# Performance work log

Hardware: AMD Instinct MI355X
Metric: run time of the kernel (lower is better)

## Reference

```python
import jax, jax.numpy as jnp
import numpy as np

STRIDE = 1
PADDING = 1  # zeros padding mode

def setup_inputs() -> dict:
    key = jax.random.key(0)
    k1, k2, k3 = jax.random.split(key, 3)
    N, C_in, H, W = 32, 128, 56, 56
    C_out, kH, kW = 256, 3, 3
    x = jax.random.normal(k1, (N, C_in, H, W), dtype=jnp.float32)
    fan_in = C_in * kH * kW
    weight = jax.random.normal(k2, (C_out, C_in, kH, kW), dtype=jnp.float32) / np.sqrt(fan_in)
    bias = jax.random.normal(k3, (C_out,), dtype=jnp.float32) * 0.01
    return {"x": x, "weight": weight, "bias": bias}

def reference(x, weight, bias):
    # Same math as the im2col unfold + GEMM: a standard 2D cross-correlation
    # with zero padding. Expressed as the fused implicit-GEMM conv primitive.
    out = jax.lax.conv_general_dilated(
        x, weight,
        window_strides=(STRIDE, STRIDE),
        padding=[(PADDING, PADDING), (PADDING, PADDING)],
        dimension_numbers=("NCHW", "OIHW", "NCHW"),
    )
    # bias broadcast over (N, C_out, H_out, W_out)
    return out + bias[None, :, None, None]
```

## Files before the change

kernel.cpp:

```cpp
#include <hip/hip_runtime.h>


typedef __attribute__((ext_vector_type(8))) short short8;
typedef __attribute__((ext_vector_type(4))) float float4v;

constexpr int NB = 32, CI = 128, HH = 56, WW = 56, CO = 256;
constexpr int HWP = HH * WW;
constexpr int HP = 58, WP = 58;
constexpr size_t XTP_BYTES = (size_t)NB * HP * WP * CI * 2;
constexpr size_t WT_OFF    = XTP_BYTES;
constexpr size_t WT_BYTES  = (size_t)9 * CO * CI * 2;
constexpr size_t WS_NEED   = WT_OFF + WT_BYTES;

__device__ inline ushort f2bf(float v) {
    union { float f; uint u; } c; c.f = v;
    uint u = c.u;
    return (ushort)((u + 0x7fffu + ((u >> 16) & 1u)) >> 16);
}

__device__ inline void gll(const ushort* g, ushort* l) {
    __builtin_amdgcn_global_load_lds(
        (const __attribute__((address_space(1))) uint*)g,
        (__attribute__((address_space(3))) uint*)l, 16, 0, 0);
}

#define BAR() do { asm volatile("" ::: "memory"); \
                   __builtin_amdgcn_s_barrier(); \
                   asm volatile("" ::: "memory"); } while (0)

__global__ __launch_bounds__(256) void xform_x(const float* __restrict__ x,
                                               ushort* __restrict__ xTp) {
    int b = blockIdx.x;
    int cit = b & 3;
    int hwt = (b >> 2) % 49;
    int n   = b / (4 * 49);
    int ci0 = cit * 32, hw0 = hwt * 64;
    __shared__ float t[32][65];
    int tx = threadIdx.x;
    int col = tx & 63, r4 = tx >> 6;
#pragma unroll
    for (int rr = 0; rr < 8; ++rr) {
        int row = rr * 4 + r4;
        t[row][col] = x[((size_t)n * CI + ci0 + row) * HWP + hw0 + col];
    }
    __syncthreads();
    int i = tx & 31, j0 = tx >> 5;
#pragma unroll
    for (int jj = 0; jj < 8; ++jj) {
        int j = jj * 8 + j0;
        int hw = hw0 + j;
        int h = hw / WW, w = hw % WW;
        xTp[(((size_t)n * HP + h + 1) * WP + (w + 1)) * CI + ci0 + i] = f2bf(t[i][j]);
    }
}

__global__ __launch_bounds__(256) void xform_border(ushort* __restrict__ xTp) {
    int u = blockIdx.x * 256 + threadIdx.x;
    int ci8 = u & 15;
    int r = u >> 4;
    int n = r / 228, bb = r % 228;
    int hp, wp;
    if (bb < 58)       { hp = 0;  wp = bb; }
    else if (bb < 116) { hp = 57; wp = bb - 58; }
    else { int c = bb - 116; hp = 1 + (c >> 1); wp = (c & 1) * 57; }
    short8 z = (short8)0;
    *reinterpret_cast<short8*>(xTp + (((size_t)n * HP + hp) * WP + wp) * CI + ci8 * 8) = z;
}

__global__ __launch_bounds__(256) void xform_w(const float* __restrict__ w,
                                               ushort* __restrict__ wT) {
    int o = blockIdx.x * 256 + threadIdx.x;
    int ci = o & 127;
    int co = (o >> 7) & 255;
    int tap = o >> 15;
    wT[o] = f2bf(w[((size_t)co * CI + ci) * 9 + tap]);
}

__global__ __launch_bounds__(512, 2) void gemm_conv(
    const ushort* __restrict__ xTp, const ushort* __restrict__ wT,
    const float* __restrict__ bias, float* __restrict__ out)
{
    __shared__ ushort As[2][256 * 64];
    __shared__ ushort Bs[2][256 * 64];

    int b = blockIdx.x;
    const int mblk = (b & 7) * 49 + (b >> 3);

    const int tid = threadIdx.x, lane = tid & 63, wv = tid >> 6;
    const int wr = wv >> 2;
    const int wc = wv & 3;

    const int s8 = (((tid & 7) ^ ((tid >> 3) & 7))) * 8;
    const int aSrc = (tid >> 3) * CI + s8;
    const int dstOff = (tid >> 3) * 64 + (tid & 7) * 8;

    int bPix[4];
#pragma unroll
    for (int hq = 0; hq < 4; ++hq) {
        int m = mblk * 256 + (hq >> 1) * 128 + (hq & 1) * 64 + (tid >> 3);
        int n = m / HWP, hw = m % HWP, h = hw / WW, w = hw % WW;
        bPix[hq] = ((n * HP + h + 1) * WP + (w + 1)) * CI + s8;
    }

    const int ck0 = (((lane >> 4)) ^ (lane & 7)) * 8;
    const int ck1 = ((4 + (lane >> 4)) ^ (lane & 7)) * 8;
    const int aRowOff = (wr * 128 + (lane & 15)) * 64;
    const int bRowOff = (wc * 64 + (lane & 15)) * 64;

    float4v acc[8][4];
#pragma unroll
    for (int i = 0; i < 8; ++i)
#pragma unroll
        for (int j = 0; j < 4; ++j) acc[i][j] = (float4v)(0.0f);

    short8 aF[4][2];
    short8 bQ0[2][2];
    short8 bQ1[2][2];

    auto STAGE_A = [&](int buf, int t, int h) {
        int tap = t >> 1, kh = (t & 1) * 64;
        const ushort* src = wT + aSrc + tap * (CO * CI) + kh + h * 16384;
        ushort* dst = &As[buf][h * 8192 + dstOff];
        gll(src, dst);
        gll(src + 8192, dst + 4096);
    };
    auto STAGE_B = [&](int buf, int t, int h) {
        int tap = t >> 1, kh = (t & 1) * 64;
        int dh = tap / 3 - 1, dw = tap % 3 - 1;
        int toff = (dh * WP + dw) * CI + kh;
        ushort* dst = &Bs[buf][h * 8192 + dstOff];
        gll(xTp + bPix[h * 2 + 0] + toff, dst);
        gll(xTp + bPix[h * 2 + 1] + toff, dst + 4096);
    };
    auto LDA = [&](int buf, int qr) {
        const ushort* p = &As[buf][aRowOff + qr * 4096];
#pragma unroll
        for (int fi = 0; fi < 4; ++fi) {
            aF[fi][0] = *(const short8*)(p + fi * 1024 + ck0);
            aF[fi][1] = *(const short8*)(p + fi * 1024 + ck1);
        }
    };
    auto LDB = [&](int buf, int qc, short8 (&bF)[2][2]) {
        const ushort* p = &Bs[buf][bRowOff + qc * 2048];
#pragma unroll
        for (int gi = 0; gi < 2; ++gi) {
            bF[gi][0] = *(const short8*)(p + gi * 1024 + ck0);
            bF[gi][1] = *(const short8*)(p + gi * 1024 + ck1);
        }
    };

#define MMQ(QR, QC, BF) do { \
    __builtin_amdgcn_s_setprio(1); \
    _Pragma("unroll") \
    for (int kc = 0; kc < 2; ++kc) \
        _Pragma("unroll") \
        for (int fi = 0; fi < 4; ++fi) \
            _Pragma("unroll") \
            for (int gi = 0; gi < 2; ++gi) \
                acc[(QR)*4+fi][(QC)*2+gi] = __builtin_amdgcn_mfma_f32_16x16x32_bf16( \
                    aF[fi][kc], (BF)[gi][kc], acc[(QR)*4+fi][(QC)*2+gi], 0, 0, 0); \
    __builtin_amdgcn_s_setprio(0); \
} while (0)

    auto TILE = [&](int c, int t) {
        LDA(c, 0);
        LDB(c, 0, bQ0);
        if (t + 1 < 18) STAGE_A(c ^ 1, t + 1, 1);
        BAR();
        MMQ(0, 0, bQ0);
        LDB(c, 1, bQ1);
        if (t + 1 < 18) STAGE_B(c ^ 1, t + 1, 1);
        BAR();
        MMQ(0, 1, bQ1);
        LDA(c, 1);
        if (t + 2 < 18) STAGE_B(c, t + 2, 0);
        BAR();
        MMQ(1, 1, bQ1);
        if (t + 2 < 18) STAGE_A(c, t + 2, 0);
        BAR();
        MMQ(1, 0, bQ0);
        if (t <= 15)      { asm volatile("s_waitcnt vmcnt(4)" ::: "memory"); }
        else if (t == 16) { asm volatile("s_waitcnt vmcnt(0)" ::: "memory"); }
        BAR();
    };

    STAGE_A(0, 0, 0); STAGE_A(0, 0, 1);
    STAGE_B(0, 0, 0); STAGE_B(0, 0, 1);
    STAGE_B(1, 1, 0); STAGE_A(1, 1, 0);
    asm volatile("s_waitcnt vmcnt(4)" ::: "memory");
    BAR();

#pragma unroll 1
    for (int tp = 0; tp < 18; tp += 2) {
        TILE(0, tp);
        TILE(1, tp + 1);
    }
#undef MMQ

    const int co0 = wr * 128;
    const int m0  = mblk * 256 + wc * 64;
    float bv[8][4];
#pragma unroll
    for (int f = 0; f < 8; ++f)
#pragma unroll
        for (int r = 0; r < 4; ++r)
            bv[f][r] = bias[co0 + f * 16 + (lane >> 4) * 4 + r];
#pragma unroll
    for (int g = 0; g < 4; ++g) {
        int m = m0 + g * 16 + (lane & 15);
        int n = m / HWP, hw = m % HWP;
        float* obase = out + (size_t)n * CO * HWP + hw;
#pragma unroll
        for (int f = 0; f < 8; ++f) {
            int co = co0 + f * 16 + (lane >> 4) * 4;
#pragma unroll
            for (int r = 0; r < 4; ++r)
                obase[(size_t)(co + r) * HWP] = acc[f][g][r] + bv[f][r];
        }
    }
}

__global__ __launch_bounds__(256) void conv_k(
    const float* __restrict__ x, const float* __restrict__ wgt,
    const float* __restrict__ bias, float* __restrict__ out)
{
    int idx = blockIdx.x * 256 + threadIdx.x;
    int wg = idx % 14; int t = idx / 14;
    int ho = t % 56; t /= 56;
    int cog = t % 64; int n = t / 64;
    int w0 = wg * 4, co0 = cog * 4;
    float acc[4][4];
#pragma unroll
    for (int j = 0; j < 4; ++j) {
        float bj = bias[co0 + j];
#pragma unroll
        for (int p = 0; p < 4; ++p) acc[j][p] = bj;
    }
    const float* xn = x + (size_t)n * CI * HWP;
    for (int ci = 0; ci < CI; ++ci) {
        float xr[3][6];
#pragma unroll
        for (int kh = 0; kh < 3; ++kh) {
            int hi = ho + kh - 1;
            if (hi >= 0 && hi < HH) {
                const float* row = xn + ((size_t)ci * HH + hi) * WW;
                float4 cc = *reinterpret_cast<const float4*>(row + w0);
                xr[kh][1] = cc.x; xr[kh][2] = cc.y; xr[kh][3] = cc.z; xr[kh][4] = cc.w;
                xr[kh][0] = (w0 > 0) ? row[w0 - 1] : 0.0f;
                xr[kh][5] = (w0 + 4 < WW) ? row[w0 + 4] : 0.0f;
            } else {
#pragma unroll
                for (int q = 0; q < 6; ++q) xr[kh][q] = 0.0f;
            }
        }
#pragma unroll
        for (int j = 0; j < 4; ++j) {
            const float* wp = wgt + ((size_t)(co0 + j) * CI + ci) * 9;
            float wvv[9];
#pragma unroll
            for (int q = 0; q < 9; ++q) wvv[q] = wp[q];
#pragma unroll
            for (int kh = 0; kh < 3; ++kh)
#pragma unroll
                for (int kw = 0; kw < 3; ++kw)
#pragma unroll
                    for (int p = 0; p < 4; ++p)
                        acc[j][p] = fmaf(xr[kh][p + kw], wvv[kh * 3 + kw], acc[j][p]);
        }
    }
#pragma unroll
    for (int j = 0; j < 4; ++j) {
        float4 v = make_float4(acc[j][0], acc[j][1], acc[j][2], acc[j][3]);
        *reinterpret_cast<float4*>(out + (((size_t)n * CO + co0 + j) * HH + ho) * WW + w0) = v;
    }
}

extern "C" void kernel_launch(void* const* d_in, const int* in_sizes, int n_in,
                              void* d_out, int out_size, void* d_ws, size_t ws_size,
                              hipStream_t stream) {
    const float* x = (const float*)d_in[0];
    const float* w = (const float*)d_in[1];
    const float* b = (const float*)d_in[2];
    float* out = (float*)d_out;

    if (ws_size < WS_NEED) {
        hipLaunchKernelGGL(conv_k, dim3(6272), dim3(256), 0, stream, x, w, b, out);
        return;
    }

    ushort* xTp = (ushort*)d_ws;
    ushort* wT  = (ushort*)((char*)d_ws + WT_OFF);

    hipLaunchKernelGGL(xform_x, dim3(32 * 49 * 4), dim3(256), 0, stream, x, xTp);
    hipLaunchKernelGGL(xform_border, dim3(456), dim3(256), 0, stream, xTp);
    hipLaunchKernelGGL(xform_w, dim3(9 * CO * CI / 256), dim3(256), 0, stream, w, wT);
    hipLaunchKernelGGL(gemm_conv, dim3(392), dim3(512), 0, stream,
                       xTp, wT, b, out);
}
```

Baseline: 95.82 us.

## Stage output tile through swizzled LDS for vectorized coalesced stores; move final MFMA after barrier

The epilogue now writes accumulators plus bias into LDS in four passes, using an XOR swizzle to avoid bank conflicts. It then reads them back as float4 rows so each thread issues 16-byte stores that are contiguous along the spatial dimension, replacing the scattered scalar stores strided by HWP. It also moves the last MFMA quarter of each tile after the vmcnt wait and barrier, which changes where the memory wait overlaps compute. The epilogue gains extra barriers and LDS traffic, and the float4 stores assume a group of four pixels never crosses an image boundary (3136 is divisible by 4).

```diff
diff --git a/kernel.cpp b/kernel.cpp
--- a/kernel.cpp
+++ b/kernel.cpp
@@ -177,11 +177,10 @@
         BAR();
         MMQ(1, 1, bQ1);
         if (t + 2 < 18) STAGE_A(c, t + 2, 0);
-        BAR();
-        MMQ(1, 0, bQ0);
         if (t <= 15)      { asm volatile("s_waitcnt vmcnt(4)" ::: "memory"); }
         else if (t == 16) { asm volatile("s_waitcnt vmcnt(0)" ::: "memory"); }
         BAR();
+        MMQ(1, 0, bQ0);
     };
 
     STAGE_A(0, 0, 0); STAGE_A(0, 0, 1);
@@ -197,25 +196,46 @@
     }
 #undef MMQ
 
-    const int co0 = wr * 128;
-    const int m0  = mblk * 256 + wc * 64;
+    const int m0  = mblk * 256;
     float bv[8][4];
 #pragma unroll
     for (int f = 0; f < 8; ++f)
 #pragma unroll
         for (int r = 0; r < 4; ++r)
-            bv[f][r] = bias[co0 + f * 16 + (lane >> 4) * 4 + r];
-#pragma unroll
-    for (int g = 0; g < 4; ++g) {
-        int m = m0 + g * 16 + (lane & 15);
-        int n = m / HWP, hw = m % HWP;
-        float* obase = out + (size_t)n * CO * HWP + hw;
-#pragma unroll
-        for (int f = 0; f < 8; ++f) {
-            int co = co0 + f * 16 + (lane >> 4) * 4;
-#pragma unroll
-            for (int r = 0; r < 4; ++r)
-                obase[(size_t)(co + r) * HWP] = acc[f][g][r] + bv[f][r];
+            bv[f][r] = bias[wr * 128 + f * 16 + (lane >> 4) * 4 + r];
+
+    float* lbuf = (float*)&As[0][0];
+    const int rd_col = tid >> 3;
+    const int rd_swz = ((rd_col ^ (rd_col >> 2)) & 3) << 3;
+
+#pragma unroll 1
+    for (int q = 0; q < 4; ++q) {
+        BAR();
+        if (wr == (q >> 1)) {
+            const int fb = 4 * (q & 1);
+#pragma unroll
+            for (int f4 = 0; f4 < 4; ++f4) {
+#pragma unroll
+                for (int r = 0; r < 4; ++r) {
+                    int co_l = f4 * 16 + (lane >> 4) * 4 + r;
+                    int swz = ((co_l ^ (co_l >> 2)) & 3) << 3;
+#pragma unroll
+                    for (int g = 0; g < 4; ++g) {
+                        int ml = wc * 64 + g * 16 + (lane & 15);
+                        lbuf[co_l * 256 + (ml ^ swz)] = acc[fb + f4][g][r] + bv[fb + f4][r];
+                    }
+                }
+            }
+        }
+        BAR();
+        const int co = q * 64 + rd_col;
+#pragma unroll
+        for (int k = 0; k < 8; ++k) {
+            int ml = ((tid & 7) + 8 * k) * 4;
+            float4v v = *(const float4v*)&lbuf[rd_col * 256 + (ml ^ rd_swz)];
+            int m = m0 + ml;
+            int n = m / HWP, hw = m % HWP;
+            *(float4v*)(out + ((size_t)n * CO + co) * HWP + hw) = v;
         }
     }
 }
```

New measurement: 148.9 us. 1.55x slower.

## Retile conv GEMM to 256x224 pixel tiles aligned to four image rows

Applied to the files above, without the earlier changes.

Changes the GEMM block tile from 256 output channels by 256 pixels to 256 by 224 pixels, where each tile covers exactly four rows of one image. The warp layout becomes 4x2 with 64x112 per-warp subtiles, so each warp holds a 4x7 accumulator array. The grid grows from 392 to 448 blocks, and B staging masks off half the threads for the last 32 rows. The intent is to spread work over more blocks on the GPU's compute units and to simplify index math, since a tile never crosses an image boundary. In exchange, per-warp operand reuse drops and the B loads become uneven across threads.

```diff
diff --git a/kernel.cpp b/kernel.cpp
--- a/kernel.cpp
+++ b/kernel.cpp
@@ -81,41 +81,43 @@
     const float* __restrict__ bias, float* __restrict__ out)
 {
     __shared__ ushort As[2][256 * 64];
-    __shared__ ushort Bs[2][256 * 64];
+    __shared__ ushort Bs[2][224 * 64];
 
     int b = blockIdx.x;
-    const int mblk = (b & 7) * 49 + (b >> 3);
+    const int mblk = (b & 7) * 56 + (b >> 3);
 
     const int tid = threadIdx.x, lane = tid & 63, wv = tid >> 6;
-    const int wr = wv >> 2;
-    const int wc = wv & 3;
+    const int wr = wv >> 1;
+    const int wc = wv & 1;
 
     const int s8 = (((tid & 7) ^ ((tid >> 3) & 7))) * 8;
     const int aSrc = (tid >> 3) * CI + s8;
     const int dstOff = (tid >> 3) * 64 + (tid & 7) * 8;
 
+    const int nimg = mblk / 14;
+    const int h0   = (mblk % 14) * 4;
     int bPix[4];
 #pragma unroll
-    for (int hq = 0; hq < 4; ++hq) {
-        int m = mblk * 256 + (hq >> 1) * 128 + (hq & 1) * 64 + (tid >> 3);
-        int n = m / HWP, hw = m % HWP, h = hw / WW, w = hw % WW;
-        bPix[hq] = ((n * HP + h + 1) * WP + (w + 1)) * CI + s8;
+    for (int p = 0; p < 4; ++p) {
+        int row = p * 64 + (tid >> 3);
+        int hh = h0 + row / 56, ww2 = row % 56;
+        bPix[p] = ((nimg * HP + hh + 1) * WP + (ww2 + 1)) * CI + s8;
     }
 
     const int ck0 = (((lane >> 4)) ^ (lane & 7)) * 8;
     const int ck1 = ((4 + (lane >> 4)) ^ (lane & 7)) * 8;
-    const int aRowOff = (wr * 128 + (lane & 15)) * 64;
-    const int bRowOff = (wc * 64 + (lane & 15)) * 64;
-
-    float4v acc[8][4];
-#pragma unroll
-    for (int i = 0; i < 8; ++i)
-#pragma unroll
-        for (int j = 0; j < 4; ++j) acc[i][j] = (float4v)(0.0f);
-
-    short8 aF[4][2];
-    short8 bQ0[2][2];
-    short8 bQ1[2][2];
+    const int aRowOff = (wr * 64 + (lane & 15)) * 64;
+    const int bRowOff = (wc * 112 + (lane & 15)) * 64;
+
+    float4v acc[4][7];
+#pragma unroll
+    for (int i = 0; i < 4; ++i)
+#pragma unroll
+        for (int j = 0; j < 7; ++j) acc[i][j] = (float4v)(0.0f);
+
+    short8 aF[2][2];
+    short8 bQ0[4][2];
+    short8 bQ1[3][2];
 
     auto STAGE_A = [&](int buf, int t, int h) {
         int tap = t >> 1, kh = (t & 1) * 64;
@@ -129,56 +131,81 @@
         int dh = tap / 3 - 1, dw = tap % 3 - 1;
         int toff = (dh * WP + dw) * CI + kh;
         ushort* dst = &Bs[buf][h * 8192 + dstOff];
-        gll(xTp + bPix[h * 2 + 0] + toff, dst);
-        gll(xTp + bPix[h * 2 + 1] + toff, dst + 4096);
+        if (h == 0) {
+            gll(xTp + bPix[0] + toff, dst);
+            gll(xTp + bPix[1] + toff, dst + 4096);
+        } else {
+            gll(xTp + bPix[2] + toff, dst);
+            if (tid < 256) gll(xTp + bPix[3] + toff, dst + 4096);
+        }
     };
     auto LDA = [&](int buf, int qr) {
-        const ushort* p = &As[buf][aRowOff + qr * 4096];
-#pragma unroll
-        for (int fi = 0; fi < 4; ++fi) {
+        const ushort* p = &As[buf][aRowOff + qr * 2048];
+#pragma unroll
+        for (int fi = 0; fi < 2; ++fi) {
             aF[fi][0] = *(const short8*)(p + fi * 1024 + ck0);
             aF[fi][1] = *(const short8*)(p + fi * 1024 + ck1);
         }
     };
-    auto LDB = [&](int buf, int qc, short8 (&bF)[2][2]) {
-        const ushort* p = &Bs[buf][bRowOff + qc * 2048];
-#pragma unroll
-        for (int gi = 0; gi < 2; ++gi) {
-            bF[gi][0] = *(const short8*)(p + gi * 1024 + ck0);
-            bF[gi][1] = *(const short8*)(p + gi * 1024 + ck1);
-        }
-    };
-
-#define MMQ(QR, QC, BF) do { \
+    auto LDB0 = [&](int buf) {
+        const ushort* p = &Bs[buf][bRowOff];
+#pragma unroll
+        for (int gi = 0; gi < 4; ++gi) {
+            bQ0[gi][0] = *(const short8*)(p + gi * 1024 + ck0);
+            bQ0[gi][1] = *(const short8*)(p + gi * 1024 + ck1);
+        }
+    };
+    auto LDB1 = [&](int buf) {
+        const ushort* p = &Bs[buf][bRowOff + 4096];
+#pragma unroll
+        for (int gi = 0; gi < 3; ++gi) {
+            bQ1[gi][0] = *(const short8*)(p + gi * 1024 + ck0);
+            bQ1[gi][1] = *(const short8*)(p + gi * 1024 + ck1);
+        }
+    };
+
+#define MMQ0(QR) do { \
     __builtin_amdgcn_s_setprio(1); \
     _Pragma("unroll") \
     for (int kc = 0; kc < 2; ++kc) \
         _Pragma("unroll") \
-        for (int fi = 0; fi < 4; ++fi) \
+        for (int fi = 0; fi < 2; ++fi) \
             _Pragma("unroll") \
-            for (int gi = 0; gi < 2; ++gi) \
-                acc[(QR)*4+fi][(QC)*2+gi] = __builtin_amdgcn_mfma_f32_16x16x32_bf16( \
-                    aF[fi][kc], (BF)[gi][kc], acc[(QR)*4+fi][(QC)*2+gi], 0, 0, 0); \
+            for (int gi = 0; gi < 4; ++gi) \
+                acc[(QR)*2+fi][gi] = __builtin_amdgcn_mfma_f32_16x16x32_bf16( \
+                    aF[fi][kc], bQ0[gi][kc], acc[(QR)*2+fi][gi], 0, 0, 0); \
     __builtin_amdgcn_s_setprio(0); \
 } while (0)
+#define MMQ1(QR) do { \
+    __builtin_amdgcn_s_setprio(1); \
+    _Pragma("unroll") \
+    for (int kc = 0; kc < 2; ++kc) \
+        _Pragma("unroll") \
+        for (int fi = 0; fi < 2; ++fi) \
+            _Pragma("unroll") \
+            for (int gi = 0; gi < 3; ++gi) \
+                acc[(QR)*2+fi][4+gi] = __builtin_amdgcn_mfma_f32_16x16x32_bf16( \
+                    aF[fi][kc], bQ1[gi][kc], acc[(QR)*2+fi][4+gi], 0, 0, 0); \
+    __builtin_amdgcn_s_setprio(0); \
+} while (0)
 
     auto TILE = [&](int c, int t) {
         LDA(c, 0);
-        LDB(c, 0, bQ0);
+        LDB0(c);
         if (t + 1 < 18) STAGE_A(c ^ 1, t + 1, 1);
         BAR();
-        MMQ(0, 0, bQ0);
-        LDB(c, 1, bQ1);
+        MMQ0(0);
+        LDB1(c);
         if (t + 1 < 18) STAGE_B(c ^ 1, t + 1, 1);
         BAR();
-        MMQ(0, 1, bQ1);
+        MMQ1(0);
         LDA(c, 1);
         if (t + 2 < 18) STAGE_B(c, t + 2, 0);
         BAR();
-        MMQ(1, 1, bQ1);
+        MMQ1(1);
         if (t + 2 < 18) STAGE_A(c, t + 2, 0);
         BAR();
-        MMQ(1, 0, bQ0);
+        MMQ0(1);
         if (t <= 15)      { asm volatile("s_waitcnt vmcnt(4)" ::: "memory"); }
         else if (t == 16) { asm volatile("s_waitcnt vmcnt(0)" ::: "memory"); }
         BAR();
@@ -195,23 +222,24 @@
         TILE(0, tp);
         TILE(1, tp + 1);
     }
-#undef MMQ
-
-    const int co0 = wr * 128;
-    const int m0  = mblk * 256 + wc * 64;
-    float bv[8][4];
-#pragma unroll
-    for (int f = 0; f < 8; ++f)
+#undef MMQ0
+#undef MMQ1
+
+    const int co0 = wr * 64;
+    const int m0  = mblk * 224 + wc * 112;
+    float bv[4][4];
+#pragma unroll
+    for (int f = 0; f < 4; ++f)
 #pragma unroll
         for (int r = 0; r < 4; ++r)
             bv[f][r] = bias[co0 + f * 16 + (lane >> 4) * 4 + r];
 #pragma unroll
-    for (int g = 0; g < 4; ++g) {
+    for (int g = 0; g < 7; ++g) {
         int m = m0 + g * 16 + (lane & 15);
-        int n = m / HWP, hw = m % HWP;
-        float* obase = out + (size_t)n * CO * HWP + hw;
-#pragma unroll
-        for (int f = 0; f < 8; ++f) {
+        int hw = m - nimg * HWP;
+        float* obase = out + (size_t)nimg * CO * HWP + hw;
+#pragma unroll
+        for (int f = 0; f < 4; ++f) {
             int co = co0 + f * 16 + (lane >> 4) * 4;
 #pragma unroll
             for (int r = 0; r < 4; ++r)
@@ -294,6 +322,6 @@
     hipLaunchKernelGGL(xform_x, dim3(32 * 49 * 4), dim3(256), 0, stream, x, xTp);
     hipLaunchKernelGGL(xform_border, dim3(456), dim3(256), 0, stream, xTp);
     hipLaunchKernelGGL(xform_w, dim3(9 * CO * CI / 256), dim3(256), 0, stream, w, wT);
-    hipLaunchKernelGGL(gemm_conv, dim3(392), dim3(512), 0, stream,
+    hipLaunchKernelGGL(gemm_conv, dim3(448), dim3(512), 0, stream,
                        xTp, wT, b, out);
 }
```

After: 88.38 us. -7.8%, faster.
